# Kernel tuning notes

Measured on AMD Instinct MI355X. Metric: run time of the kernel, lower is better.

## Reference

```python
import jax, jax.numpy as jnp
import numpy as np

B, N, D, H = 2, 64, 256, 8
DK = D // H
EPS = 1e-5


def layer_norm(x, g, b):
    mu = jnp.mean(x, axis=-1, keepdims=True)
    var = jnp.var(x, axis=-1, keepdims=True)
    return (x - mu) * jax.lax.rsqrt(var + EPS) * g + b


def setup_inputs() -> dict:
    key = jax.random.key(0)
    ks = jax.random.split(key, 12)
    s = 1.0 / np.sqrt(D)
    inp = {
        "x": jax.random.normal(ks[0], (B, N, N, D), jnp.float32),
        "W_lk": jax.random.uniform(ks[1], (D, D), jnp.float32, -s, s),
        "W_rk": jax.random.uniform(ks[2], (D, D), jnp.float32, -s, s),
        "W_lv": jax.random.uniform(ks[3], (D, D), jnp.float32, -s, s),
        "W_rv": jax.random.uniform(ks[4], (D, D), jnp.float32, -s, s),
        "W_out": jax.random.uniform(ks[5], (D, D), jnp.float32, -s, s),
        "ln_agg_g": jnp.ones((D,), jnp.float32),
        "ln_agg_b": jnp.zeros((D,), jnp.float32),
        "W1": jax.random.uniform(ks[6], (D, 2 * D), jnp.float32, -s, s),
        "b1": jnp.zeros((2 * D,), jnp.float32),
        "W2": jax.random.uniform(ks[7], (2 * D, D), jnp.float32, -1.0 / np.sqrt(2 * D), 1.0 / np.sqrt(2 * D)),
        "b2": jnp.zeros((D,), jnp.float32),
        "ln2_g": jnp.ones((D,), jnp.float32),
        "ln2_b": jnp.zeros((D,), jnp.float32),
    }
    return inp


def reference(x, W_lk, W_rk, W_lv, W_rv, W_out, ln_agg_g, ln_agg_b, W1, b1, W2, b2, ln2_g, ln2_b):
    b, n = x.shape[0], x.shape[1]
    # projections (no bias), split into heads: [b, n, n, H, DK]
    lk = (x @ W_lk).reshape(b, n, n, H, DK)
    rk = (x @ W_rk).reshape(b, n, n, H, DK)
    lv = (x @ W_lv).reshape(b, n, n, H, DK)
    rv = (x @ W_rv).reshape(b, n, n, H, DK)
    # triangle attention scores over intermediate node 'a'
    scores = jnp.einsum('bxahd,bayhd->bxayh', lk, rk) / np.sqrt(DK)
    att = jax.nn.softmax(scores, axis=2)
    # fused triangle value aggregation: sum_a att * lv[x,a] * rv[a,y]
    o = jnp.einsum('bxayh,bxahd,bayhd->bxyhd', att, lv, rv)
    o = o.reshape(b, n, n, D) @ W_out
    # FFN block (dropout = 0)
    h = layer_norm(x + o, ln_agg_g, ln_agg_b)
    m = jax.nn.relu(h @ W1 + b1) @ W2 + b2
    return layer_norm(m + h, ln2_g, ln2_b)
```

## Files before the change

### kernel.cpp

```cpp
#include <hip/hip_runtime.h>

#define ROWS 8192
#define DIM  256

typedef short short8 __attribute__((ext_vector_type(8)));
typedef float f4     __attribute__((ext_vector_type(4)));

__device__ __forceinline__ float bf2f(unsigned int u16) {
    union { unsigned int i; float f; } v;
    v.i = (u16 & 0xffffu) << 16;
    return v.f;
}
__device__ __forceinline__ unsigned short f2bf(float f) {
    union { float f; unsigned int u; } v; v.f = f;
    unsigned int r = v.u + 0x7fffu + ((v.u >> 16) & 1u);
    return (unsigned short)(r >> 16);
}

__global__ __launch_bounds__(256)
void cast_all(const float* __restrict__ x, unsigned short* __restrict__ xb,
              const float* __restrict__ w0, const float* __restrict__ w1,
              const float* __restrict__ w2, const float* __restrict__ w3,
              const float* __restrict__ w4, const float* __restrict__ w5,
              const float* __restrict__ w6, unsigned short* __restrict__ wt)
{
    if (blockIdx.x < 2048) {
        const size_t i = ((size_t)blockIdx.x * 256 + threadIdx.x) * 4;
        float4 v = *(const float4*)(x + i);
        uint2 p;
        p.x = f2bf(v.x) | ((unsigned int)f2bf(v.y) << 16);
        p.y = f2bf(v.z) | ((unsigned int)f2bf(v.w) << 16);
        *(uint2*)(xb + i) = p;
        return;
    }
    __shared__ float t[32][33];
    int id = blockIdx.x - 2048;
    const float* src; int K, N, Ntiles; size_t doff;
    if (id < 320) {
        int w = id >> 6; id &= 63; K = 256; N = 256; Ntiles = 8;
        doff = (size_t)w * 65536;
        src = (w == 0) ? w0 : (w == 1) ? w1 : (w == 2) ? w2 : (w == 3) ? w3 : w4;
    } else if (id < 448) {
        id -= 320; K = 256; N = 512; Ntiles = 16; doff = 327680; src = w5;
    } else {
        id -= 448; K = 512; N = 256; Ntiles = 8;  doff = 458752; src = w6;
    }
    const int tk = id / Ntiles, tn = id % Ntiles;
    const int k0 = tk * 32, n0 = tn * 32;
    const int c = threadIdx.x & 31, r8 = threadIdx.x >> 5;
    for (int rr = r8; rr < 32; rr += 8)
        t[rr][c] = src[(size_t)(k0 + rr) * N + n0 + c];
    __syncthreads();
    for (int rr = r8; rr < 32; rr += 8)
        wt[doff + (size_t)(n0 + rr) * K + k0 + c] = f2bf(t[c][rr]);
}

__global__ __launch_bounds__(256)
void proj_mfma(const unsigned short* __restrict__ A, const unsigned short* __restrict__ WT,
               unsigned short* __restrict__ projT)
{
    const int lane = threadIdx.x & 63, wave = threadIdx.x >> 6;
    const int wsel = blockIdx.x >> 2;
    const int col0 = (blockIdx.x & 3) * 64;
    const int m0 = blockIdx.y * 128 + wave * 32;
    const int lm = lane & 15, lk8 = (lane >> 4) * 8;
    const unsigned short* W = WT + (size_t)wsel * 65536;
    unsigned short* dst = projT + (size_t)wsel * 2097152;

    f4 acc[2][4];
    #pragma unroll
    for (int i = 0; i < 2; ++i)
        #pragma unroll
        for (int j = 0; j < 4; ++j) acc[i][j] = (f4){0.f, 0.f, 0.f, 0.f};

    for (int kc = 0; kc < 256; kc += 32) {
        short8 af[2], bf[4];
        #pragma unroll
        for (int i = 0; i < 2; ++i)
            af[i] = *(const short8*)(A + (size_t)(m0 + i * 16 + lm) * 256 + kc + lk8);
        #pragma unroll
        for (int j = 0; j < 4; ++j)
            bf[j] = *(const short8*)(W + (size_t)(col0 + j * 16 + lm) * 256 + kc + lk8);
        #pragma unroll
        for (int i = 0; i < 2; ++i)
            #pragma unroll
            for (int j = 0; j < 4; ++j)
                acc[i][j] = __builtin_amdgcn_mfma_f32_16x16x32_bf16(af[i], bf[j], acc[i][j], 0, 0, 0);
    }

    const int rbase = (lane >> 4) * 4;
    const int swap = (wsel == 3);
    #pragma unroll
    for (int i = 0; i < 2; ++i)
        #pragma unroll
        for (int j = 0; j < 4; ++j) {
            const int c = col0 + j * 16 + lm;
            const int h = c >> 5, d = c & 31;
            #pragma unroll
            for (int r = 0; r < 4; ++r) {
                const int m = m0 + i * 16 + rbase + r;
                const int b = m >> 12, ii = (m >> 6) & 63, jj = m & 63;
                const int p = swap ? jj : ii;
                const int q = swap ? ii : jj;
                const size_t idx = ((((size_t)b * 8 + h) * 64 + p) * 64 + q) * 32 + d;
                dst[idx] = f2bf(acc[i][j][r]);
            }
        }
}

__global__ __launch_bounds__(256)
void scores_mfma(const unsigned short* __restrict__ lkT, const unsigned short* __restrict__ rkT,
                 unsigned short* __restrict__ S)
{
    const int lane = threadIdx.x & 63, wave = threadIdx.x >> 6;
    const int bi = blockIdx.x;
    const int b = bi >> 7, h = (bi >> 4) & 7, a = (bi & 15) * 4 + wave;
    const size_t bh = (size_t)b * 8 + h;
    const int lm = lane & 15, lk8 = (lane >> 4) * 8;

    short8 af[4], bf[4];
    #pragma unroll
    for (int t = 0; t < 4; ++t) {
        af[t] = *(const short8*)(lkT + ((bh * 64 + (t * 16 + lm)) * 64 + a) * 32 + lk8);
        bf[t] = *(const short8*)(rkT + ((bh * 64 + a) * 64 + (t * 16 + lm)) * 32 + lk8);
    }
    const int rbase = (lane >> 4) * 4;
    unsigned short* Sb = S + bh * 262144 + a * 64;
    #pragma unroll
    for (int mt = 0; mt < 4; ++mt)
        #pragma unroll
        for (int nt = 0; nt < 4; ++nt) {
            f4 acc = (f4){0.f, 0.f, 0.f, 0.f};
            acc = __builtin_amdgcn_mfma_f32_16x16x32_bf16(af[mt], bf[nt], acc, 0, 0, 0);
            #pragma unroll
            for (int r = 0; r < 4; ++r) {
                const int xx = mt * 16 + rbase + r;
                const int yy = nt * 16 + lm;
                Sb[(size_t)xx * 4096 + yy] = f2bf(acc[r] * 0.17677669529663687f);
            }
        }
}

__global__ __launch_bounds__(256)
void softmax_agg(const unsigned short* __restrict__ S, const unsigned short* __restrict__ lvT,
                 const unsigned short* __restrict__ rvT, unsigned short* __restrict__ obuf)
{
    __shared__ float att[64][64];
    __shared__ float lvL[64][32];
    __shared__ float smx[4][64], ssm[4][64], invL[64];
    const int bi = blockIdx.x;
    const int b = bi >> 9, h = (bi >> 6) & 7, x = bi & 63;
    const size_t bh = (size_t)b * 8 + h;
    const int tid = threadIdx.x;

    {
        const int a = tid >> 2, yo = (tid & 3) * 16;
        const unsigned short* Sp = S + (bh * 64 + x) * 4096 + a * 64 + yo;
        uint4 p0 = *(const uint4*)(Sp);
        uint4 p1 = *(const uint4*)(Sp + 8);
        att[a][yo +  0] = bf2f(p0.x); att[a][yo +  1] = bf2f(p0.x >> 16);
        att[a][yo +  2] = bf2f(p0.y); att[a][yo +  3] = bf2f(p0.y >> 16);
        att[a][yo +  4] = bf2f(p0.z); att[a][yo +  5] = bf2f(p0.z >> 16);
        att[a][yo +  6] = bf2f(p0.w); att[a][yo +  7] = bf2f(p0.w >> 16);
        att[a][yo +  8] = bf2f(p1.x); att[a][yo +  9] = bf2f(p1.x >> 16);
        att[a][yo + 10] = bf2f(p1.y); att[a][yo + 11] = bf2f(p1.y >> 16);
        att[a][yo + 12] = bf2f(p1.z); att[a][yo + 13] = bf2f(p1.z >> 16);
        att[a][yo + 14] = bf2f(p1.w); att[a][yo + 15] = bf2f(p1.w >> 16);
        const int d0 = (tid & 3) * 8;
        uint4 q = *(const uint4*)(lvT + ((bh * 64 + x) * 64 + a) * 32 + d0);
        lvL[a][d0 + 0] = bf2f(q.x); lvL[a][d0 + 1] = bf2f(q.x >> 16);
        lvL[a][d0 + 2] = bf2f(q.y); lvL[a][d0 + 3] = bf2f(q.y >> 16);
        lvL[a][d0 + 4] = bf2f(q.z); lvL[a][d0 + 5] = bf2f(q.z >> 16);
        lvL[a][d0 + 6] = bf2f(q.w); lvL[a][d0 + 7] = bf2f(q.w >> 16);
    }
    __syncthreads();

    {
        const int y = tid & 63, az = tid >> 6;
        float mx = -1e30f;
        for (int a = az; a < 64; a += 4) mx = fmaxf(mx, att[a][y]);
        smx[az][y] = mx;
    }
    __syncthreads();

    {
        const int y = tid & 63, az = tid >> 6;
        const float mx = fmaxf(fmaxf(smx[0][y], smx[1][y]), fmaxf(smx[2][y], smx[3][y]));
        float s = 0.f;
        for (int a = az; a < 64; a += 4) {
            float e = __expf(att[a][y] - mx);
            att[a][y] = e;
            s += e;
        }
        ssm[az][y] = s;
    }
    __syncthreads();
    if (tid < 64)
        invL[tid] = 1.f / (ssm[0][tid] + ssm[1][tid] + ssm[2][tid] + ssm[3][tid]);
    __syncthreads();

    {
        const int dp = tid & 15, yb = tid >> 4;
        #pragma unroll
        for (int it = 0; it < 4; ++it) {
            const int y = yb + it * 16;
            const unsigned short* rvr = rvT + (bh * 64 + y) * 2048 + dp * 2;
            float a0 = 0.f, a1 = 0.f;
            #pragma unroll 8
            for (int a = 0; a < 64; ++a) {
                unsigned int pk = *(const unsigned int*)(rvr + a * 32);
                float w = att[a][y];
                a0 += w * lvL[a][2 * dp]     * bf2f(pk);
                a1 += w * lvL[a][2 * dp + 1] * bf2f(pk >> 16);
            }
            const float inv = invL[y];
            a0 *= inv; a1 *= inv;
            unsigned int st = f2bf(a0) | ((unsigned int)f2bf(a1) << 16);
            *(unsigned int*)(obuf + (((size_t)b * 64 + x) * 64 + y) * 256 + h * 32 + dp * 2) = st;
        }
    }
}

__global__ __launch_bounds__(256)
void gemm_mfma(const unsigned short* __restrict__ A, const unsigned short* __restrict__ WT,
               const float* __restrict__ bias, unsigned short* __restrict__ outB,
               int K, int N)
{
    const int lane = threadIdx.x & 63, wave = threadIdx.x >> 6;
    const int m0 = blockIdx.y * 128 + wave * 32;
    const int col0 = blockIdx.x * 64;
    const int lm = lane & 15, lk8 = (lane >> 4) * 8;

    f4 acc[2][4];
    #pragma unroll
    for (int i = 0; i < 2; ++i)
        #pragma unroll
        for (int j = 0; j < 4; ++j) acc[i][j] = (f4){0.f, 0.f, 0.f, 0.f};

    for (int kc = 0; kc < K; kc += 32) {
        short8 af[2], bf[4];
        #pragma unroll
        for (int i = 0; i < 2; ++i)
            af[i] = *(const short8*)(A + (size_t)(m0 + i * 16 + lm) * K + kc + lk8);
        #pragma unroll
        for (int j = 0; j < 4; ++j)
            bf[j] = *(const short8*)(WT + (size_t)(col0 + j * 16 + lm) * K + kc + lk8);
        #pragma unroll
        for (int i = 0; i < 2; ++i)
            #pragma unroll
            for (int j = 0; j < 4; ++j)
                acc[i][j] = __builtin_amdgcn_mfma_f32_16x16x32_bf16(af[i], bf[j], acc[i][j], 0, 0, 0);
    }

    const int rbase = (lane >> 4) * 4;
    #pragma unroll
    for (int i = 0; i < 2; ++i)
        #pragma unroll
        for (int j = 0; j < 4; ++j) {
            const int n = col0 + j * 16 + lm;
            const float bb = bias[n];
            #pragma unroll
            for (int r = 0; r < 4; ++r) {
                const int m = m0 + i * 16 + rbase + r;
                outB[(size_t)m * N + n] = f2bf(fmaxf(acc[i][j][r] + bb, 0.f));
            }
        }
}

__global__ __launch_bounds__(256)
void gemm_ln(const unsigned short* __restrict__ A, const unsigned short* __restrict__ WT,
             const float* __restrict__ bias, const float* __restrict__ resid,
             const float* __restrict__ gamma, const float* __restrict__ beta,
             float* __restrict__ outF, unsigned short* __restrict__ outB,
             int K, int mode)
{
    __shared__ float ps[16][4], pq[16][4];
    const int lane = threadIdx.x & 63, wave = threadIdx.x >> 6;
    const int m0 = blockIdx.x * 16;
    const int col0 = wave * 64;
    const int lm = lane & 15, lk8 = (lane >> 4) * 8;

    f4 acc[4];
    #pragma unroll
    for (int j = 0; j < 4; ++j) acc[j] = (f4){0.f, 0.f, 0.f, 0.f};

    for (int kc = 0; kc < K; kc += 32) {
        short8 af = *(const short8*)(A + (size_t)(m0 + lm) * K + kc + lk8);
        #pragma unroll
        for (int j = 0; j < 4; ++j) {
            short8 bf = *(const short8*)(WT + (size_t)(col0 + j * 16 + lm) * K + kc + lk8);
            acc[j] = __builtin_amdgcn_mfma_f32_16x16x32_bf16(af, bf, acc[j], 0, 0, 0);
        }
    }

    const int rbase = (lane >> 4) * 4;
    float v[4][4];
    float s[4] = {0.f, 0.f, 0.f, 0.f}, q[4] = {0.f, 0.f, 0.f, 0.f};
    #pragma unroll
    for (int j = 0; j < 4; ++j) {
        const int n = col0 + j * 16 + lm;
        const float bb = bias ? bias[n] : 0.f;
        #pragma unroll
        for (int r = 0; r < 4; ++r) {
            const int m = m0 + rbase + r;
            float t = acc[j][r] + bb + resid[(size_t)m * 256 + n];
            v[j][r] = t;
            s[r] += t;
            q[r] += t * t;
        }
    }
    #pragma unroll
    for (int off = 1; off < 16; off <<= 1) {
        #pragma unroll
        for (int r = 0; r < 4; ++r) {
            s[r] += __shfl_xor(s[r], off);
            q[r] += __shfl_xor(q[r], off);
        }
    }
    if (lm == 0) {
        #pragma unroll
        for (int r = 0; r < 4; ++r) {
            ps[rbase + r][wave] = s[r];
            pq[rbase + r][wave] = q[r];
        }
    }
    __syncthreads();
    #pragma unroll
    for (int r = 0; r < 4; ++r) {
        const int lr = rbase + r;
        const float Sm = ps[lr][0] + ps[lr][1] + ps[lr][2] + ps[lr][3];
        const float Qm = pq[lr][0] + pq[lr][1] + pq[lr][2] + pq[lr][3];
        const float mu = Sm * (1.f / 256.f);
        const float ri = rsqrtf(Qm * (1.f / 256.f) - mu * mu + 1e-5f);
        const int m = m0 + lr;
        #pragma unroll
        for (int j = 0; j < 4; ++j) {
            const int n = col0 + j * 16 + lm;
            const float rv = (v[j][r] - mu) * ri * gamma[n] + beta[n];
            outF[(size_t)m * 256 + n] = rv;
            if (mode == 0) outB[(size_t)m * 256 + n] = f2bf(rv);
        }
    }
}

extern "C" void kernel_launch(void* const* d_in, const int* in_sizes, int n_in,
                              void* d_out, int out_size, void* d_ws, size_t ws_size,
                              hipStream_t stream)
{
    const float* x    = (const float*)d_in[0];
    const float* Wlk  = (const float*)d_in[1];
    const float* Wrk  = (const float*)d_in[2];
    const float* Wlv  = (const float*)d_in[3];
    const float* Wrv  = (const float*)d_in[4];
    const float* Wout = (const float*)d_in[5];
    const float* g1   = (const float*)d_in[6];
    const float* be1  = (const float*)d_in[7];
    const float* W1   = (const float*)d_in[8];
    const float* b1   = (const float*)d_in[9];
    const float* W2   = (const float*)d_in[10];
    const float* b2   = (const float*)d_in[11];
    const float* g2   = (const float*)d_in[12];
    const float* be2  = (const float*)d_in[13];

    char* base = (char*)d_ws;
    const size_t MB = 1ull << 20;
    unsigned short* xb    = (unsigned short*)(base + 0);
    unsigned short* obufb = (unsigned short*)(base + 0);
    unsigned short* projT = (unsigned short*)(base + 4 * MB);
    unsigned short* lkT   = projT;
    unsigned short* rkT   = projT + 2097152;
    unsigned short* lvT   = projT + 2 * 2097152;
    unsigned short* rvT   = projT + 3 * 2097152;
    float*          hf    = (float*)(base + 20 * MB);
    unsigned short* hb    = (unsigned short*)(base + 28 * MB);
    unsigned short* midb  = (unsigned short*)(base + 36 * MB);
    unsigned short* Sbuf  = (unsigned short*)(base + 44 * MB);
    unsigned short* WT    = (unsigned short*)(base + 52 * MB);

    cast_all<<<2624, 256, 0, stream>>>(x, xb, Wlk, Wrk, Wlv, Wrv, Wout, W1, W2, WT);
    proj_mfma<<<dim3(16, 64), 256, 0, stream>>>(xb, WT, projT);
    scores_mfma<<<256, 256, 0, stream>>>(lkT, rkT, Sbuf);
    softmax_agg<<<1024, 256, 0, stream>>>(Sbuf, lvT, rvT, obufb);
    gemm_ln<<<512, 256, 0, stream>>>(obufb, WT + 262144, nullptr, x, g1, be1, hf, hb, 256, 0);
    gemm_mfma<<<dim3(8, 64), 256, 0, stream>>>(hb, WT + 327680, b1, midb, 256, 512);
    gemm_ln<<<512, 256, 0, stream>>>(midb, WT + 458752, b2, hf, g2, be2, (float*)d_out, nullptr, 512, 1);
}
```

Measured before the change: 193.9 us.

## Fuse FFN into one kernel, store lv/rv as fp32, vectorize aggregation

The two FFN GEMMs and the second layernorm are fused into one kernel that keeps the 512-wide hidden activations in shared memory, removing the mid-buffer round trip and one launch. lv and rv are now written as fp32 so the aggregation loop can use float4 loads, and each thread computes 8 output dims with vectorized reads instead of strided 2-element bf16 reads. The residual for the final layernorm is read from the bf16 copy of h instead of an fp32 copy, which slightly lowers precision. Some loops also gain unroll pragmas.

```diff
diff --git a/kernel.cpp b/kernel.cpp
--- a/kernel.cpp
+++ b/kernel.cpp
@@ -57,7 +57,8 @@
 
 __global__ __launch_bounds__(256)
 void proj_mfma(const unsigned short* __restrict__ A, const unsigned short* __restrict__ WT,
-               unsigned short* __restrict__ projT)
+               unsigned short* __restrict__ lkT, unsigned short* __restrict__ rkT,
+               float* __restrict__ lvF, float* __restrict__ rvF)
 {
     const int lane = threadIdx.x & 63, wave = threadIdx.x >> 6;
     const int wsel = blockIdx.x >> 2;
@@ -65,7 +66,6 @@
     const int m0 = blockIdx.y * 128 + wave * 32;
     const int lm = lane & 15, lk8 = (lane >> 4) * 8;
     const unsigned short* W = WT + (size_t)wsel * 65536;
-    unsigned short* dst = projT + (size_t)wsel * 2097152;
 
     f4 acc[2][4];
     #pragma unroll
@@ -73,6 +73,7 @@
         #pragma unroll
         for (int j = 0; j < 4; ++j) acc[i][j] = (f4){0.f, 0.f, 0.f, 0.f};
 
+    #pragma unroll 2
     for (int kc = 0; kc < 256; kc += 32) {
         short8 af[2], bf[4];
         #pragma unroll
@@ -103,7 +104,11 @@
                 const int p = swap ? jj : ii;
                 const int q = swap ? ii : jj;
                 const size_t idx = ((((size_t)b * 8 + h) * 64 + p) * 64 + q) * 32 + d;
-                dst[idx] = f2bf(acc[i][j][r]);
+                const float v = acc[i][j][r];
+                if      (wsel == 0) lkT[idx] = f2bf(v);
+                else if (wsel == 1) rkT[idx] = f2bf(v);
+                else if (wsel == 2) lvF[idx] = v;
+                else                rvF[idx] = v;
             }
         }
 }
@@ -142,8 +147,8 @@
 }
 
 __global__ __launch_bounds__(256)
-void softmax_agg(const unsigned short* __restrict__ S, const unsigned short* __restrict__ lvT,
-                 const unsigned short* __restrict__ rvT, unsigned short* __restrict__ obuf)
+void softmax_agg(const unsigned short* __restrict__ S, const float* __restrict__ lvF,
+                 const float* __restrict__ rvF, unsigned short* __restrict__ obuf)
 {
     __shared__ float att[64][64];
     __shared__ float lvL[64][32];
@@ -167,11 +172,9 @@
         att[a][yo + 12] = bf2f(p1.z); att[a][yo + 13] = bf2f(p1.z >> 16);
         att[a][yo + 14] = bf2f(p1.w); att[a][yo + 15] = bf2f(p1.w >> 16);
         const int d0 = (tid & 3) * 8;
-        uint4 q = *(const uint4*)(lvT + ((bh * 64 + x) * 64 + a) * 32 + d0);
-        lvL[a][d0 + 0] = bf2f(q.x); lvL[a][d0 + 1] = bf2f(q.x >> 16);
-        lvL[a][d0 + 2] = bf2f(q.y); lvL[a][d0 + 3] = bf2f(q.y >> 16);
-        lvL[a][d0 + 4] = bf2f(q.z); lvL[a][d0 + 5] = bf2f(q.z >> 16);
-        lvL[a][d0 + 6] = bf2f(q.w); lvL[a][d0 + 7] = bf2f(q.w >> 16);
+        const float* lvp = lvF + ((bh * 64 + x) * 64 + a) * 32 + d0;
+        *(float4*)&lvL[a][d0]     = *(const float4*)(lvp);
+        *(float4*)&lvL[a][d0 + 4] = *(const float4*)(lvp + 4);
     }
     __syncthreads();
 
@@ -200,80 +203,43 @@
     __syncthreads();
 
     {
-        const int dp = tid & 15, yb = tid >> 4;
-        #pragma unroll
-        for (int it = 0; it < 4; ++it) {
-            const int y = yb + it * 16;
-            const unsigned short* rvr = rvT + (bh * 64 + y) * 2048 + dp * 2;
-            float a0 = 0.f, a1 = 0.f;
-            #pragma unroll 8
-            for (int a = 0; a < 64; ++a) {
-                unsigned int pk = *(const unsigned int*)(rvr + a * 32);
-                float w = att[a][y];
-                a0 += w * lvL[a][2 * dp]     * bf2f(pk);
-                a1 += w * lvL[a][2 * dp + 1] * bf2f(pk >> 16);
-            }
-            const float inv = invL[y];
-            a0 *= inv; a1 *= inv;
-            unsigned int st = f2bf(a0) | ((unsigned int)f2bf(a1) << 16);
-            *(unsigned int*)(obuf + (((size_t)b * 64 + x) * 64 + y) * 256 + h * 32 + dp * 2) = st;
-        }
-    }
-}
-
-__global__ __launch_bounds__(256)
-void gemm_mfma(const unsigned short* __restrict__ A, const unsigned short* __restrict__ WT,
-               const float* __restrict__ bias, unsigned short* __restrict__ outB,
-               int K, int N)
-{
-    const int lane = threadIdx.x & 63, wave = threadIdx.x >> 6;
-    const int m0 = blockIdx.y * 128 + wave * 32;
-    const int col0 = blockIdx.x * 64;
-    const int lm = lane & 15, lk8 = (lane >> 4) * 8;
-
-    f4 acc[2][4];
-    #pragma unroll
-    for (int i = 0; i < 2; ++i)
-        #pragma unroll
-        for (int j = 0; j < 4; ++j) acc[i][j] = (f4){0.f, 0.f, 0.f, 0.f};
-
-    for (int kc = 0; kc < K; kc += 32) {
-        short8 af[2], bf[4];
-        #pragma unroll
-        for (int i = 0; i < 2; ++i)
-            af[i] = *(const short8*)(A + (size_t)(m0 + i * 16 + lm) * K + kc + lk8);
-        #pragma unroll
-        for (int j = 0; j < 4; ++j)
-            bf[j] = *(const short8*)(WT + (size_t)(col0 + j * 16 + lm) * K + kc + lk8);
-        #pragma unroll
-        for (int i = 0; i < 2; ++i)
-            #pragma unroll
-            for (int j = 0; j < 4; ++j)
-                acc[i][j] = __builtin_amdgcn_mfma_f32_16x16x32_bf16(af[i], bf[j], acc[i][j], 0, 0, 0);
-    }
-
-    const int rbase = (lane >> 4) * 4;
-    #pragma unroll
-    for (int i = 0; i < 2; ++i)
-        #pragma unroll
-        for (int j = 0; j < 4; ++j) {
-            const int n = col0 + j * 16 + lm;
-            const float bb = bias[n];
-            #pragma unroll
-            for (int r = 0; r < 4; ++r) {
-                const int m = m0 + i * 16 + rbase + r;
-                outB[(size_t)m * N + n] = f2bf(fmaxf(acc[i][j][r] + bb, 0.f));
-            }
-        }
-}
-
-__global__ __launch_bounds__(256)
-void gemm_ln(const unsigned short* __restrict__ A, const unsigned short* __restrict__ WT,
-             const float* __restrict__ bias, const float* __restrict__ resid,
-             const float* __restrict__ gamma, const float* __restrict__ beta,
-             float* __restrict__ outF, unsigned short* __restrict__ outB,
-             int K, int mode)
-{
+        const int y = tid >> 2, d0 = (tid & 3) * 8;
+        float o[8];
+        #pragma unroll
+        for (int i = 0; i < 8; ++i) o[i] = 0.f;
+        const float* rvr = rvF + (bh * 64 + y) * 2048 + d0;
+        for (int a = 0; a < 64; ++a) {
+            const float w = att[a][y];
+            float4 lv0 = *(const float4*)&lvL[a][d0];
+            float4 lv1 = *(const float4*)&lvL[a][d0 + 4];
+            float4 rv0 = *(const float4*)(rvr + (size_t)a * 32);
+            float4 rv1 = *(const float4*)(rvr + (size_t)a * 32 + 4);
+            o[0] = fmaf(w * lv0.x, rv0.x, o[0]);
+            o[1] = fmaf(w * lv0.y, rv0.y, o[1]);
+            o[2] = fmaf(w * lv0.z, rv0.z, o[2]);
+            o[3] = fmaf(w * lv0.w, rv0.w, o[3]);
+            o[4] = fmaf(w * lv1.x, rv1.x, o[4]);
+            o[5] = fmaf(w * lv1.y, rv1.y, o[5]);
+            o[6] = fmaf(w * lv1.z, rv1.z, o[6]);
+            o[7] = fmaf(w * lv1.w, rv1.w, o[7]);
+        }
+        const float inv = invL[y];
+        uint4 pk;
+        pk.x = f2bf(o[0] * inv) | ((unsigned int)f2bf(o[1] * inv) << 16);
+        pk.y = f2bf(o[2] * inv) | ((unsigned int)f2bf(o[3] * inv) << 16);
+        pk.z = f2bf(o[4] * inv) | ((unsigned int)f2bf(o[5] * inv) << 16);
+        pk.w = f2bf(o[6] * inv) | ((unsigned int)f2bf(o[7] * inv) << 16);
+        *(uint4*)(obuf + (((size_t)b * 64 + x) * 64 + y) * 256 + h * 32 + d0) = pk;
+    }
+}
+
+__global__ __launch_bounds__(256)
+void gemm_ln1(const unsigned short* __restrict__ A, const unsigned short* __restrict__ WT,
+              const float* __restrict__ resid,
+              const float* __restrict__ gamma, const float* __restrict__ beta,
+              unsigned short* __restrict__ out)
+{
+    constexpr int K = 256;
     __shared__ float ps[16][4], pq[16][4];
     const int lane = threadIdx.x & 63, wave = threadIdx.x >> 6;
     const int m0 = blockIdx.x * 16;
@@ -284,6 +250,7 @@
     #pragma unroll
     for (int j = 0; j < 4; ++j) acc[j] = (f4){0.f, 0.f, 0.f, 0.f};
 
+    #pragma unroll 2
     for (int kc = 0; kc < K; kc += 32) {
         short8 af = *(const short8*)(A + (size_t)(m0 + lm) * K + kc + lk8);
         #pragma unroll
@@ -299,14 +266,13 @@
     #pragma unroll
     for (int j = 0; j < 4; ++j) {
         const int n = col0 + j * 16 + lm;
-        const float bb = bias ? bias[n] : 0.f;
         #pragma unroll
         for (int r = 0; r < 4; ++r) {
             const int m = m0 + rbase + r;
-            float t = acc[j][r] + bb + resid[(size_t)m * 256 + n];
+            float t = acc[j][r] + resid[(size_t)m * 256 + n];
             v[j][r] = t;
             s[r] += t;
-            q[r] += t * t;
+            q[r] = fmaf(t, t, q[r]);
         }
     }
     #pragma unroll
@@ -336,9 +302,102 @@
         #pragma unroll
         for (int j = 0; j < 4; ++j) {
             const int n = col0 + j * 16 + lm;
-            const float rv = (v[j][r] - mu) * ri * gamma[n] + beta[n];
-            outF[(size_t)m * 256 + n] = rv;
-            if (mode == 0) outB[(size_t)m * 256 + n] = f2bf(rv);
+            out[(size_t)m * 256 + n] = f2bf((v[j][r] - mu) * ri * gamma[n] + beta[n]);
+        }
+    }
+}
+
+__global__ __launch_bounds__(256)
+void ffn_fused(const unsigned short* __restrict__ hb, const unsigned short* __restrict__ WT1,
+               const float* __restrict__ b1, const unsigned short* __restrict__ WT2,
+               const float* __restrict__ b2, const float* __restrict__ gamma,
+               const float* __restrict__ beta, float* __restrict__ out)
+{
+    __shared__ unsigned short mid[16][520];
+    __shared__ float ps[16][4], pq[16][4];
+    const int lane = threadIdx.x & 63, wave = threadIdx.x >> 6;
+    const int m0 = blockIdx.x * 16;
+    const int lm = lane & 15, lk8 = (lane >> 4) * 8;
+    const int rbase = (lane >> 4) * 4;
+
+    short8 af[8];
+    #pragma unroll
+    for (int kc = 0; kc < 8; ++kc)
+        af[kc] = *(const short8*)(hb + (size_t)(m0 + lm) * 256 + kc * 32 + lk8);
+    const int colb = wave * 128;
+    #pragma unroll
+    for (int j = 0; j < 8; ++j) {
+        const int n = colb + j * 16 + lm;
+        f4 acc = (f4){0.f, 0.f, 0.f, 0.f};
+        #pragma unroll
+        for (int kc = 0; kc < 8; ++kc) {
+            short8 bf = *(const short8*)(WT1 + (size_t)n * 256 + kc * 32 + lk8);
+            acc = __builtin_amdgcn_mfma_f32_16x16x32_bf16(af[kc], bf, acc, 0, 0, 0);
+        }
+        const float bb = b1[n];
+        #pragma unroll
+        for (int r = 0; r < 4; ++r)
+            mid[rbase + r][n] = f2bf(fmaxf(acc[r] + bb, 0.f));
+    }
+    __syncthreads();
+
+    const int col0 = wave * 64;
+    f4 acc2[4];
+    #pragma unroll
+    for (int j = 0; j < 4; ++j) acc2[j] = (f4){0.f, 0.f, 0.f, 0.f};
+    #pragma unroll 4
+    for (int kc = 0; kc < 16; ++kc) {
+        short8 a2 = *(const short8*)&mid[lm][kc * 32 + lk8];
+        #pragma unroll
+        for (int j = 0; j < 4; ++j) {
+            short8 bf = *(const short8*)(WT2 + (size_t)(col0 + j * 16 + lm) * 512 + kc * 32 + lk8);
+            acc2[j] = __builtin_amdgcn_mfma_f32_16x16x32_bf16(a2, bf, acc2[j], 0, 0, 0);
+        }
+    }
+
+    float v[4][4];
+    float s[4] = {0.f, 0.f, 0.f, 0.f}, q[4] = {0.f, 0.f, 0.f, 0.f};
+    #pragma unroll
+    for (int j = 0; j < 4; ++j) {
+        const int n = col0 + j * 16 + lm;
+        const float bb = b2[n];
+        #pragma unroll
+        for (int r = 0; r < 4; ++r) {
+            const int m = m0 + rbase + r;
+            float t = acc2[j][r] + bb + bf2f(hb[(size_t)m * 256 + n]);
+            v[j][r] = t;
+            s[r] += t;
+            q[r] = fmaf(t, t, q[r]);
+        }
+    }
+    #pragma unroll
+    for (int off = 1; off < 16; off <<= 1) {
+        #pragma unroll
+        for (int r = 0; r < 4; ++r) {
+            s[r] += __shfl_xor(s[r], off);
+            q[r] += __shfl_xor(q[r], off);
+        }
+    }
+    if (lm == 0) {
+        #pragma unroll
+        for (int r = 0; r < 4; ++r) {
+            ps[rbase + r][wave] = s[r];
+            pq[rbase + r][wave] = q[r];
+        }
+    }
+    __syncthreads();
+    #pragma unroll
+    for (int r = 0; r < 4; ++r) {
+        const int lr = rbase + r;
+        const float Sm = ps[lr][0] + ps[lr][1] + ps[lr][2] + ps[lr][3];
+        const float Qm = pq[lr][0] + pq[lr][1] + pq[lr][2] + pq[lr][3];
+        const float mu = Sm * (1.f / 256.f);
+        const float ri = rsqrtf(Qm * (1.f / 256.f) - mu * mu + 1e-5f);
+        const int m = m0 + lr;
+        #pragma unroll
+        for (int j = 0; j < 4; ++j) {
+            const int n = col0 + j * 16 + lm;
+            out[(size_t)m * 256 + n] = (v[j][r] - mu) * ri * gamma[n] + beta[n];
         }
     }
 }
@@ -366,22 +425,18 @@
     const size_t MB = 1ull << 20;
     unsigned short* xb    = (unsigned short*)(base + 0);
     unsigned short* obufb = (unsigned short*)(base + 0);
-    unsigned short* projT = (unsigned short*)(base + 4 * MB);
-    unsigned short* lkT   = projT;
-    unsigned short* rkT   = projT + 2097152;
-    unsigned short* lvT   = projT + 2 * 2097152;
-    unsigned short* rvT   = projT + 3 * 2097152;
-    float*          hf    = (float*)(base + 20 * MB);
-    unsigned short* hb    = (unsigned short*)(base + 28 * MB);
-    unsigned short* midb  = (unsigned short*)(base + 36 * MB);
+    unsigned short* lkT   = (unsigned short*)(base + 4 * MB);
+    unsigned short* hb    = (unsigned short*)(base + 4 * MB);
+    unsigned short* rkT   = (unsigned short*)(base + 8 * MB);
+    float*          lvF   = (float*)(base + 12 * MB);
+    float*          rvF   = (float*)(base + 28 * MB);
     unsigned short* Sbuf  = (unsigned short*)(base + 44 * MB);
     unsigned short* WT    = (unsigned short*)(base + 52 * MB);
 
     cast_all<<<2624, 256, 0, stream>>>(x, xb, Wlk, Wrk, Wlv, Wrv, Wout, W1, W2, WT);
-    proj_mfma<<<dim3(16, 64), 256, 0, stream>>>(xb, WT, projT);
+    proj_mfma<<<dim3(16, 64), 256, 0, stream>>>(xb, WT, lkT, rkT, lvF, rvF);
     scores_mfma<<<256, 256, 0, stream>>>(lkT, rkT, Sbuf);
-    softmax_agg<<<1024, 256, 0, stream>>>(Sbuf, lvT, rvT, obufb);
-    gemm_ln<<<512, 256, 0, stream>>>(obufb, WT + 262144, nullptr, x, g1, be1, hf, hb, 256, 0);
-    gemm_mfma<<<dim3(8, 64), 256, 0, stream>>>(hb, WT + 327680, b1, midb, 256, 512);
-    gemm_ln<<<512, 256, 0, stream>>>(midb, WT + 458752, b2, hf, g2, be2, (float*)d_out, nullptr, 512, 1);
-}
+    softmax_agg<<<1024, 256, 0, stream>>>(Sbuf, lvF, rvF, obufb);
+    gemm_ln1<<<512, 256, 0, stream>>>(obufb, WT + 262144, x, g1, be1, hb);
+    ffn_fused<<<512, 256, 0, stream>>>(hb, WT + 327680, b1, WT + 458752, b2, g2, be2, (float*)d_out);
+}
```

After: 193.8 us. Within noise of the previous version (-0.0%).
